# Kernel optimization log

Measured on AMD Instinct MI355X. Metric: run time of the kernel, lower is better.

## Reference

```python
import jax, jax.numpy as jnp
import numpy as np

EPS = 1e-3  # keras LayerNormalization default epsilon


def layer_norm(x, gamma, beta):
    mu = jnp.mean(x, axis=-1, keepdims=True)
    var = jnp.var(x, axis=-1, keepdims=True)
    return (x - mu) * jax.lax.rsqrt(var + EPS) * gamma + beta


def setup_inputs() -> dict:
    key = jax.random.key(0)
    ks = jax.random.split(key, 16)
    B, S, D = 8, 2048, 1024          # batch, seq, input_size
    P = 2 * D                        # up-projection dim (proj_factor=2)
    H = 1024                         # hidden = head_size(64) * num_heads(16)
    s = 0.02
    inp = {
        "x": jax.random.normal(ks[0], (B, S, D), jnp.float32),
        "ln1_g": jnp.ones((D,), jnp.float32),
        "ln1_b": jnp.zeros((D,), jnp.float32),
        "W_up": jax.random.normal(ks[1], (D, P), jnp.float32) * s,
        "b_up": jnp.zeros((P,), jnp.float32),
        "W_adj": jax.random.normal(ks[2], (P, H), jnp.float32) * s,
        "b_adj": jnp.zeros((H,), jnp.float32),
        "W_q": jax.random.normal(ks[3], (H, H), jnp.float32) * s,
        "b_q": jnp.zeros((H,), jnp.float32),
        "W_k": jax.random.normal(ks[4], (H, H), jnp.float32) * s,
        "b_k": jnp.zeros((H,), jnp.float32),
        "W_v": jax.random.normal(ks[5], (H, H), jnp.float32) * s,
        "b_v": jnp.zeros((H,), jnp.float32),
        "W_i": jax.random.normal(ks[6], (H, H), jnp.float32) * s,
        "b_i": jnp.zeros((H,), jnp.float32),
        "W_f": jax.random.normal(ks[7], (H, H), jnp.float32) * s,
        "b_f": jnp.zeros((H,), jnp.float32),
        "W_o": jax.random.normal(ks[8], (H, H), jnp.float32) * s,
        "b_o": jnp.zeros((H,), jnp.float32),
        "ln2_g": jnp.ones((H,), jnp.float32),
        "ln2_b": jnpos if False else jnp.zeros((H,), jnp.float32),
        "W_down": jax.random.normal(ks[9], (H, D), jnp.float32) * s,
        "b_down": jnp.zeros((D,), jnp.float32),
    }
    return inp


def reference(x, ln1_g, ln1_b, W_up, b_up, W_adj, b_adj,
              W_q, b_q, W_k, b_k, W_v, b_v,
              W_i, b_i, W_f, b_f, W_o, b_o,
              ln2_g, ln2_b, W_down, b_down):
    head_size = 64
    x_norm = layer_norm(x, ln1_g, ln1_b)
    x_up = x_norm @ W_up + b_up                      # [B,S,2D]
    x_adj = x_up @ W_adj + b_adj                     # [B,S,H]
    # BlockDiagonal layers: each block is a Dense over the FULL input,
    # concatenated -> equivalent to one [H,H] matmul with concatenated weights.
    q = x_adj @ W_q + b_q
    k = (x_adj @ W_k + b_k) / (head_size ** 0.5)
    v = x_adj @ W_v + b_v
    i_t = x_adj @ W_i + b_i
    f_t = x_adj @ W_f + b_f
    o = jax.nn.sigmoid(x_adj @ W_o + b_o)
    m_t = jnp.maximum(f_t, i_t)
    f = jnp.exp(f_t - m_t)                           # (i = exp(i_t - m_t) unused downstream)
    c_t = f * v * k
    h_t = o * (c_t * q) / jnp.maximum(jnp.abs(k * q), 1.0)
    out = layer_norm(h_t, ln2_g, ln2_b) * jax.nn.sigmoid(x_adj)
    out = out @ W_down + b_down
    return out + x
```

## Files before the change

kernel.cpp:

```cpp
#include <hip/hip_runtime.h>


typedef unsigned short u16;
typedef __attribute__((ext_vector_type(4))) unsigned short u16x4;
typedef __attribute__((ext_vector_type(8))) unsigned short u16x8;
typedef __attribute__((ext_vector_type(8))) __bf16 bf16x8;
typedef __attribute__((ext_vector_type(4))) float f32x4;

__device__ __forceinline__ float bf2f(u16 u) {
    union { unsigned int i; float f; } c; c.i = ((unsigned int)u) << 16; return c.f;
}
__device__ __forceinline__ u16 f2bf(float f) {
    union { float f; unsigned int i; } c; c.f = f;
    unsigned int lsb = (c.i >> 16) & 1u;
    c.i += 0x7fffu + lsb;
    return (u16)(c.i >> 16);
}
__device__ __forceinline__ float sigmoidf(float z) {
    return 1.0f / (1.0f + __expf(-z));
}

#define GLDS16(gp, lp)                                                        \
    __builtin_amdgcn_global_load_lds(                                         \
        (__attribute__((address_space(1))) void*)(void*)(gp),                 \
        (__attribute__((address_space(3))) void*)(lp), 16, 0, 0)

#define BM 128
#define BN 128
#define BK 32

template <int MODE>
__global__ __launch_bounds__(256) void gemm_bt(
    const u16* __restrict__ A, const u16* __restrict__ Bt,
    const float* __restrict__ bias, const float* __restrict__ resid,
    void* __restrict__ out, int M, int N, int K, float scale)
{
    __shared__ __align__(16) u16 As[2 * BM * BK];
    __shared__ __align__(16) u16 Bs[2 * BN * BK];

    const int tid  = threadIdx.x;
    const int lane = tid & 63;
    const int wave = tid >> 6;
    const int l15  = lane & 15;
    const int quad = lane >> 4;

    const long bm = (long)blockIdx.y * BM;
    const long bn = (long)blockIdx.x * BN;
    const int  wm = (wave >> 1) * 64;
    const int  wn = (wave & 1) * 64;

    f32x4 acc[4][4] = {};

    const int  r0 = tid >> 2;
    const int  ck = (((tid & 3) ^ ((tid >> 3) & 3)) * 8);
    const u16* ga0 = A  + (bm + r0) * (long)K + ck;
    const u16* gb0 = Bt + (bn + r0) * (long)K + ck;
    const int  ldst = wave * 512;

    auto stage = [&](int t_, int b_) {
        const long kof = (long)t_ * BK;
        u16* dA = &As[b_ * (BM * BK) + ldst];
        u16* dB = &Bs[b_ * (BN * BK) + ldst];
        GLDS16(ga0 + kof, dA);
        GLDS16(ga0 + kof + 64 * (long)K, dA + 2048);
        GLDS16(gb0 + kof, dB);
        GLDS16(gb0 + kof + 64 * (long)K, dB + 2048);
    };

    const int q8s = (quad ^ ((l15 >> 1) & 3)) * 8;
    const int nk  = K / BK;

    stage(0, 0);
    stage(1, 1);

    for (int t = 0; t < nk; ++t) {
        const int cur = t & 1;
        if (t + 1 < nk) asm volatile("s_waitcnt vmcnt(4)" ::: "memory");
        else            asm volatile("s_waitcnt vmcnt(0)" ::: "memory");
        __builtin_amdgcn_s_barrier();

        bf16x8 af[4], bfr[4];
#pragma unroll
        for (int t4 = 0; t4 < 4; ++t4) {
            af[t4]  = *(const bf16x8*)&As[cur * (BM * BK) + (wm + t4 * 16 + l15) * BK + q8s];
            bfr[t4] = *(const bf16x8*)&Bs[cur * (BN * BK) + (wn + t4 * 16 + l15) * BK + q8s];
        }
        asm volatile("s_waitcnt lgkmcnt(0)" ::: "memory");
        __builtin_amdgcn_s_barrier();
        if (t + 2 < nk) stage(t + 2, cur);

#pragma unroll
        for (int mt = 0; mt < 4; ++mt)
#pragma unroll
            for (int nt = 0; nt < 4; ++nt)
                acc[mt][nt] = __builtin_amdgcn_mfma_f32_16x16x32_bf16(
                    af[mt], bfr[nt], acc[mt][nt], 0, 0, 0);
    }

#pragma unroll
    for (int nt = 0; nt < 4; ++nt) {
        const long n  = bn + wn + nt * 16 + l15;
        const float bv = (MODE == 2) ? 0.0f : bias[n];
#pragma unroll
        for (int mt = 0; mt < 4; ++mt) {
            const long m0 = bm + wm + mt * 16 + quad * 4;
#pragma unroll
            for (int r = 0; r < 4; ++r) {
                const long idx = (m0 + r) * N + n;
                const float val = (acc[mt][nt][r] + bv) * scale;
                if (MODE == 1) ((float*)out)[idx] = val + resid[idx];
                else           ((u16*)out)[idx] = f2bf(val);
            }
        }
    }
}

__global__ __launch_bounds__(256) void gemm_gates(
    const u16* __restrict__ A, const u16* __restrict__ Wcat,
    const float* __restrict__ bq_, const float* __restrict__ bk_,
    const float* __restrict__ bv_, const float* __restrict__ bi_,
    const float* __restrict__ bf_, const float* __restrict__ bo_,
    u16* __restrict__ ht, int M, int N, int K)
{
    __shared__ __align__(16) u16 As[2 * 128 * 64];
    __shared__ __align__(16) u16 Bs[2 * 6 * 32 * 64];

    const int tid  = threadIdx.x;
    const int lane = tid & 63;
    const int wave = tid >> 6;
    const int l15  = lane & 15;
    const int quad = lane >> 4;

    const long bm = (long)blockIdx.y * 128;
    const long bn = (long)blockIdx.x * 32;

    f32x4 acc[6][4] = {};

    const int  rr = lane >> 3;
    const int  ck = (((lane & 7) ^ rr) * 8);

    const u16* gaj[4];
    int lAo[4];
#pragma unroll
    for (int j = 0; j < 4; ++j) {
        const int c = wave * 4 + j;
        gaj[j] = A + (bm + c * 8 + rr) * (long)K + ck;
        lAo[j] = c * 512;
    }
    const u16* gbj[6];
    int lBo[6];
#pragma unroll
    for (int j = 0; j < 6; ++j) {
        const int c = wave * 6 + j;
        const int g = c >> 2;
        const int r = (c & 3) * 8 + rr;
        gbj[j] = Wcat + ((long)g * 1024 + bn + r) * (long)K + ck;
        lBo[j] = c * 512;
    }

    auto stage = [&](int t_, int b_) {
        const long kof = (long)t_ * 64;
#pragma unroll
        for (int j = 0; j < 4; ++j)
            GLDS16(gaj[j] + kof, &As[b_ * 8192 + lAo[j]]);
#pragma unroll
        for (int j = 0; j < 6; ++j)
            GLDS16(gbj[j] + kof, &Bs[b_ * 12288 + lBo[j]]);
    };

    const int mh = (wave >> 1) * 64;
    const int nb = (wave & 1) * 16;
    const int l7 = l15 & 7;
    const int nk = K >> 6;

    stage(0, 0);
    stage(1, 1);

    for (int t = 0; t < nk; ++t) {
        const int cur = t & 1;
        if (t + 1 < nk) asm volatile("s_waitcnt vmcnt(10)" ::: "memory");
        else            asm volatile("s_waitcnt vmcnt(0)"  ::: "memory");
        __builtin_amdgcn_s_barrier();

        const int ab = cur * 8192;
        const int bb = cur * 12288;

        {
            const int so = (quad ^ l7) * 8;
            bf16x8 af[4];
#pragma unroll
            for (int t4 = 0; t4 < 4; ++t4)
                af[t4] = *(const bf16x8*)&As[ab + (mh + t4 * 16 + l15) * 64 + so];
#pragma unroll
            for (int g = 0; g < 6; ++g) {
                const bf16x8 bfrag =
                    *(const bf16x8*)&Bs[bb + (g * 32 + nb + l15) * 64 + so];
#pragma unroll
                for (int t4 = 0; t4 < 4; ++t4)
                    acc[g][t4] = __builtin_amdgcn_mfma_f32_16x16x32_bf16(
                        af[t4], bfrag, acc[g][t4], 0, 0, 0);
            }
        }
        bf16x8 af1[4], bf1[6];
        {
            const int so = ((4 + quad) ^ l7) * 8;
#pragma unroll
            for (int t4 = 0; t4 < 4; ++t4)
                af1[t4] = *(const bf16x8*)&As[ab + (mh + t4 * 16 + l15) * 64 + so];
#pragma unroll
            for (int g = 0; g < 6; ++g)
                bf1[g] = *(const bf16x8*)&Bs[bb + (g * 32 + nb + l15) * 64 + so];
        }
        asm volatile("s_waitcnt lgkmcnt(0)" ::: "memory");
        __builtin_amdgcn_s_barrier();
        if (t + 2 < nk) stage(t + 2, cur);

#pragma unroll
        for (int g = 0; g < 6; ++g)
#pragma unroll
            for (int t4 = 0; t4 < 4; ++t4)
                acc[g][t4] = __builtin_amdgcn_mfma_f32_16x16x32_bf16(
                    af1[t4], bf1[g], acc[g][t4], 0, 0, 0);
    }

    const long n = bn + nb + l15;
    const float bqn = bq_[n], bkn = bk_[n], bvn = bv_[n];
    const float bin = bi_[n], bfn = bf_[n], bon = bo_[n];
#pragma unroll
    for (int t = 0; t < 4; ++t) {
        const long m0 = bm + mh + t * 16 + quad * 4;
#pragma unroll
        for (int r = 0; r < 4; ++r) {
            const float qf = acc[0][t][r] + bqn;
            const float kf = (acc[1][t][r] + bkn) * 0.125f;
            const float vf = acc[2][t][r] + bvn;
            const float fi = acc[3][t][r] + bin;
            const float ff = acc[4][t][r] + bfn;
            const float osig = sigmoidf(acc[5][t][r] + bon);
            const float mx = fmaxf(ff, fi);
            const float fe = __expf(ff - mx);
            const float ct = fe * vf * kf;
            const float h  = osig * (ct * qf) / fmaxf(fabsf(kf * qf), 1.0f);
            ht[(m0 + r) * N + n] = f2bf(h);
        }
    }
}

__global__ __launch_bounds__(256) void ln_in_kernel(
    const float* __restrict__ x, const float* __restrict__ g,
    const float* __restrict__ b, u16* __restrict__ xn)
{
    const long row = blockIdx.x;
    const int  tid = threadIdx.x;
    const float4 v = ((const float4*)(x + row * 1024))[tid];
    float s  = v.x + v.y + v.z + v.w;
    float s2 = v.x * v.x + v.y * v.y + v.z * v.z + v.w * v.w;
#pragma unroll
    for (int off = 32; off > 0; off >>= 1) {
        s  += __shfl_down(s, off);
        s2 += __shfl_down(s2, off);
    }
    __shared__ float red[8];
    const int wave = tid >> 6;
    if ((tid & 63) == 0) { red[wave] = s; red[4 + wave] = s2; }
    __syncthreads();
    if (tid == 0) {
        const float S  = red[0] + red[1] + red[2] + red[3];
        const float S2 = red[4] + red[5] + red[6] + red[7];
        const float mu = S * (1.0f / 1024.0f);
        const float var = S2 * (1.0f / 1024.0f) - mu * mu;
        red[0] = mu; red[1] = rsqrtf(var + 1e-3f);
    }
    __syncthreads();
    const float mu = red[0], rstd = red[1];
    const int c = tid * 4;
    u16x4 o;
    o.x = f2bf((v.x - mu) * rstd * g[c + 0] + b[c + 0]);
    o.y = f2bf((v.y - mu) * rstd * g[c + 1] + b[c + 1]);
    o.z = f2bf((v.z - mu) * rstd * g[c + 2] + b[c + 2]);
    o.w = f2bf((v.w - mu) * rstd * g[c + 3] + b[c + 3]);
    *(u16x4*)(xn + row * 1024 + c) = o;
}

__global__ __launch_bounds__(256) void convT_kernel(
    const float* __restrict__ W, u16* __restrict__ Wt, int K, int N)
{
    __shared__ float t[32][33];
    const int tx = threadIdx.x & 31;
    const int ty = threadIdx.x >> 5;
    const long bn = (long)blockIdx.x * 32;
    const long bk = (long)blockIdx.y * 32;
#pragma unroll
    for (int j = 0; j < 4; ++j)
        t[ty + j * 8][tx] = W[(bk + ty + j * 8) * N + bn + tx];
    __syncthreads();
#pragma unroll
    for (int j = 0; j < 4; ++j)
        Wt[(bn + ty + j * 8) * K + bk + tx] = f2bf(t[tx][ty + j * 8]);
}

__global__ __launch_bounds__(256) void convB_kernel(
    const float* __restrict__ W, u16* __restrict__ Wb)
{
    const long i = ((long)blockIdx.x * 256 + threadIdx.x) * 4;
    const float4 v = *(const float4*)(W + i);
    u16x4 o;
    o.x = f2bf(v.x); o.y = f2bf(v.y); o.z = f2bf(v.z); o.w = f2bf(v.w);
    *(u16x4*)(Wb + i) = o;
}

__global__ __launch_bounds__(256) void bcomb_kernel(
    const u16* __restrict__ WadjT, const float* __restrict__ bup,
    const float* __restrict__ badj, float* __restrict__ bcomb)
{
    const long h = blockIdx.x;
    const int  tid = threadIdx.x;
    const int  p = tid * 8;
    const u16x8 w = *(const u16x8*)&WadjT[h * 2048 + p];
    float s = 0.0f;
#pragma unroll
    for (int j = 0; j < 8; ++j) s += bf2f(w[j]) * bup[p + j];
#pragma unroll
    for (int off = 32; off > 0; off >>= 1) s += __shfl_down(s, off);
    __shared__ float red[4];
    const int wave = tid >> 6;
    if ((tid & 63) == 0) red[wave] = s;
    __syncthreads();
    if (tid == 0)
        bcomb[h] = red[0] + red[1] + red[2] + red[3] + badj[h];
}

__global__ __launch_bounds__(256) void ln2_kernel(
    const u16* __restrict__ ht, const u16* __restrict__ xadj,
    const float* __restrict__ g2, const float* __restrict__ b2,
    u16* __restrict__ y)
{
    const long base = (long)blockIdx.x * 1024;
    const int  tid = threadIdx.x;
    const int  c = tid * 4;
    const u16x4 hv = *(const u16x4*)&ht[base + c];
    const u16x4 xv = *(const u16x4*)&xadj[base + c];

    float h[4];
    float s = 0.0f, s2 = 0.0f;
#pragma unroll
    for (int j = 0; j < 4; ++j) {
        h[j] = bf2f(hv[j]);
        s += h[j]; s2 += h[j] * h[j];
    }
#pragma unroll
    for (int off = 32; off > 0; off >>= 1) {
        s  += __shfl_down(s, off);
        s2 += __shfl_down(s2, off);
    }
    __shared__ float red[8];
    const int wave = tid >> 6;
    if ((tid & 63) == 0) { red[wave] = s; red[4 + wave] = s2; }
    __syncthreads();
    if (tid == 0) {
        const float S  = red[0] + red[1] + red[2] + red[3];
        const float S2 = red[4] + red[5] + red[6] + red[7];
        const float mu = S * (1.0f / 1024.0f);
        const float var = S2 * (1.0f / 1024.0f) - mu * mu;
        red[0] = mu; red[1] = rsqrtf(var + 1e-3f);
    }
    __syncthreads();
    const float mu = red[0], rstd = red[1];
    u16x4 o;
#pragma unroll
    for (int j = 0; j < 4; ++j)
        o[j] = f2bf(((h[j] - mu) * rstd * g2[c + j] + b2[c + j]) * sigmoidf(bf2f(xv[j])));
    *(u16x4*)&y[base + c] = o;
}

extern "C" void kernel_launch(void* const* d_in, const int* in_sizes, int n_in,
                              void* d_out, int out_size, void* d_ws, size_t ws_size,
                              hipStream_t stream)
{
    const float* x    = (const float*)d_in[0];
    const float* g1   = (const float*)d_in[1];
    const float* b1   = (const float*)d_in[2];
    const float* Wup  = (const float*)d_in[3];
    const float* bup  = (const float*)d_in[4];
    const float* Wadj = (const float*)d_in[5];
    const float* badj = (const float*)d_in[6];
    const float* Wq = (const float*)d_in[7];   const float* bq = (const float*)d_in[8];
    const float* Wk = (const float*)d_in[9];   const float* bk = (const float*)d_in[10];
    const float* Wv = (const float*)d_in[11];  const float* bv = (const float*)d_in[12];
    const float* Wi = (const float*)d_in[13];  const float* bi = (const float*)d_in[14];
    const float* Wf = (const float*)d_in[15];  const float* bf = (const float*)d_in[16];
    const float* Wo = (const float*)d_in[17];  const float* bo = (const float*)d_in[18];
    const float* g2 = (const float*)d_in[19];  const float* b2 = (const float*)d_in[20];
    const float* Wdn = (const float*)d_in[21]; const float* bdn = (const float*)d_in[22];

    const int M = 8 * 2048;
    const int D = 1024, P = 2048, H = 1024;

    char* ws = (char*)d_ws;
    const size_t MB = 1024 * 1024;
    u16* xn     = (u16*)(ws + 0);
    u16* htb    = (u16*)(ws + 0);
    u16* yb     = (u16*)(ws + 0);
    u16* WcombT = (u16*)(ws + 32 * MB);
    float* bcomb = (float*)(ws + 36 * MB);
    u16* xadj   = (u16*)(ws + 96 * MB);
    u16* Wup_bf = (u16*)(ws + 128 * MB);
    u16* WadjT  = (u16*)(ws + 132 * MB);
    u16* Wcat   = (u16*)(ws + 136 * MB);
    u16* WdnT   = (u16*)(ws + 148 * MB);

    ln_in_kernel<<<M, 256, 0, stream>>>(x, g1, b1, xn);

    convB_kernel<<<(D * P) / (256 * 4), 256, 0, stream>>>(Wup, Wup_bf);
    convT_kernel<<<dim3(H / 32, P / 32), 256, 0, stream>>>(Wadj, WadjT, P, H);
    convT_kernel<<<dim3(H / 32, H / 32), 256, 0, stream>>>(Wq, Wcat + 0 * H * H, H, H);
    convT_kernel<<<dim3(H / 32, H / 32), 256, 0, stream>>>(Wk, Wcat + 1 * H * H, H, H);
    convT_kernel<<<dim3(H / 32, H / 32), 256, 0, stream>>>(Wv, Wcat + 2 * H * H, H, H);
    convT_kernel<<<dim3(H / 32, H / 32), 256, 0, stream>>>(Wi, Wcat + 3 * H * H, H, H);
    convT_kernel<<<dim3(H / 32, H / 32), 256, 0, stream>>>(Wf, Wcat + 4 * H * H, H, H);
    convT_kernel<<<dim3(H / 32, H / 32), 256, 0, stream>>>(Wo, Wcat + 5 * H * H, H, H);
    convT_kernel<<<dim3(D / 32, H / 32), 256, 0, stream>>>(Wdn, WdnT, H, D);
    bcomb_kernel<<<H, 256, 0, stream>>>(WadjT, bup, badj, bcomb);

    gemm_bt<2><<<dim3(D / BN, H / BM), 256, 0, stream>>>(
        WadjT, Wup_bf, nullptr, nullptr, WcombT, H, D, P, 1.0f);

    gemm_bt<0><<<dim3(H / BN, M / BM), 256, 0, stream>>>(
        xn, WcombT, bcomb, nullptr, xadj, M, H, D, 1.0f);

    gemm_gates<<<dim3(H / 32, M / 128), 256, 0, stream>>>(
        xadj, Wcat, bq, bk, bv, bi, bf, bo, htb, M, H, H);

    ln2_kernel<<<M, 256, 0, stream>>>(htb, xadj, g2, b2, yb);

    gemm_bt<1><<<dim3(D / BN, M / BM), 256, 0, stream>>>(yb, WdnT, bdn, x, (float*)d_out, M, D, H, 1.0f);
}
```

Measured before the change: 569.1 us.

## Merge weight prep kernels into one launch and raise wave priority around MFMA loops

```diff
diff --git a/kernel.cpp b/kernel.cpp
--- a/kernel.cpp
+++ b/kernel.cpp
@@ -89,12 +89,14 @@
         __builtin_amdgcn_s_barrier();
         if (t + 2 < nk) stage(t + 2, cur);
 
+        __builtin_amdgcn_s_setprio(1);
 #pragma unroll
         for (int mt = 0; mt < 4; ++mt)
 #pragma unroll
             for (int nt = 0; nt < 4; ++nt)
                 acc[mt][nt] = __builtin_amdgcn_mfma_f32_16x16x32_bf16(
                     af[mt], bfr[nt], acc[mt][nt], 0, 0, 0);
+        __builtin_amdgcn_s_setprio(0);
     }
 
 #pragma unroll
@@ -191,6 +193,7 @@
 #pragma unroll
             for (int t4 = 0; t4 < 4; ++t4)
                 af[t4] = *(const bf16x8*)&As[ab + (mh + t4 * 16 + l15) * 64 + so];
+            __builtin_amdgcn_s_setprio(1);
 #pragma unroll
             for (int g = 0; g < 6; ++g) {
                 const bf16x8 bfrag =
@@ -200,6 +203,7 @@
                     acc[g][t4] = __builtin_amdgcn_mfma_f32_16x16x32_bf16(
                         af[t4], bfrag, acc[g][t4], 0, 0, 0);
             }
+            __builtin_amdgcn_s_setprio(0);
         }
         bf16x8 af1[4], bf1[6];
         {
@@ -215,12 +219,14 @@
         __builtin_amdgcn_s_barrier();
         if (t + 2 < nk) stage(t + 2, cur);
 
+        __builtin_amdgcn_s_setprio(1);
 #pragma unroll
         for (int g = 0; g < 6; ++g)
 #pragma unroll
             for (int t4 = 0; t4 < 4; ++t4)
                 acc[g][t4] = __builtin_amdgcn_mfma_f32_16x16x32_bf16(
                     af1[t4], bf1[g], acc[g][t4], 0, 0, 0);
+        __builtin_amdgcn_s_setprio(0);
     }
 
     const long n = bn + nb + l15;
@@ -282,14 +288,21 @@
     *(u16x4*)(xn + row * 1024 + c) = o;
 }
 
-__global__ __launch_bounds__(256) void convT_kernel(
-    const float* __restrict__ W, u16* __restrict__ Wt, int K, int N)
-{
-    __shared__ float t[32][33];
+struct PrepArgs {
+    const float *Wadj, *Wq, *Wk, *Wv, *Wi, *Wf, *Wo, *Wdn, *Wup;
+    const float *bup, *badj;
+    u16 *WadjT, *Wcat, *WdnT, *Wup_bf;
+    float *bcomb;
+};
+
+__device__ __forceinline__ void do_transpose(
+    const float* __restrict__ W, u16* __restrict__ Wt,
+    int K, int N, int bx, int by, float (&t)[32][33])
+{
     const int tx = threadIdx.x & 31;
     const int ty = threadIdx.x >> 5;
-    const long bn = (long)blockIdx.x * 32;
-    const long bk = (long)blockIdx.y * 32;
+    const long bn = (long)bx * 32;
+    const long bk = (long)by * 32;
 #pragma unroll
     for (int j = 0; j < 4; ++j)
         t[ty + j * 8][tx] = W[(bk + ty + j * 8) * N + bn + tx];
@@ -299,35 +312,46 @@
         Wt[(bn + ty + j * 8) * K + bk + tx] = f2bf(t[tx][ty + j * 8]);
 }
 
-__global__ __launch_bounds__(256) void convB_kernel(
-    const float* __restrict__ W, u16* __restrict__ Wb)
-{
-    const long i = ((long)blockIdx.x * 256 + threadIdx.x) * 4;
-    const float4 v = *(const float4*)(W + i);
-    u16x4 o;
-    o.x = f2bf(v.x); o.y = f2bf(v.y); o.z = f2bf(v.z); o.w = f2bf(v.w);
-    *(u16x4*)(Wb + i) = o;
-}
-
-__global__ __launch_bounds__(256) void bcomb_kernel(
-    const u16* __restrict__ WadjT, const float* __restrict__ bup,
-    const float* __restrict__ badj, float* __restrict__ bcomb)
-{
-    const long h = blockIdx.x;
-    const int  tid = threadIdx.x;
-    const int  p = tid * 8;
-    const u16x8 w = *(const u16x8*)&WadjT[h * 2048 + p];
-    float s = 0.0f;
-#pragma unroll
-    for (int j = 0; j < 8; ++j) s += bf2f(w[j]) * bup[p + j];
-#pragma unroll
-    for (int off = 32; off > 0; off >>= 1) s += __shfl_down(s, off);
-    __shared__ float red[4];
-    const int wave = tid >> 6;
-    if ((tid & 63) == 0) red[wave] = s;
-    __syncthreads();
-    if (tid == 0)
-        bcomb[h] = red[0] + red[1] + red[2] + red[3] + badj[h];
+__global__ __launch_bounds__(256) void prep_kernel(PrepArgs a)
+{
+    __shared__ float t[32][33];
+    int bid = blockIdx.x;
+    if (bid < 2048) {
+        do_transpose(a.Wadj, a.WadjT, 2048, 1024, bid & 31, bid >> 5, t);
+        return;
+    }
+    bid -= 2048;
+    if (bid < 6144) {
+        const int g = bid >> 10, tt = bid & 1023;
+        const float* Wg = g == 0 ? a.Wq : g == 1 ? a.Wk : g == 2 ? a.Wv
+                        : g == 3 ? a.Wi : g == 4 ? a.Wf : a.Wo;
+        do_transpose(Wg, a.Wcat + (long)g * 1024 * 1024, 1024, 1024,
+                     tt & 31, tt >> 5, t);
+        return;
+    }
+    bid -= 6144;
+    if (bid < 1024) {
+        do_transpose(a.Wdn, a.WdnT, 1024, 1024, bid & 31, bid >> 5, t);
+        return;
+    }
+    bid -= 1024;
+    if (bid < 2048) {
+        const long i = ((long)bid * 256 + threadIdx.x) * 4;
+        const float4 v = *(const float4*)(a.Wup + i);
+        u16x4 o;
+        o.x = f2bf(v.x); o.y = f2bf(v.y); o.z = f2bf(v.z); o.w = f2bf(v.w);
+        *(u16x4*)(a.Wup_bf + i) = o;
+        return;
+    }
+    bid -= 2048;
+    {
+        const int h = bid * 256 + threadIdx.x;
+        float s = 0.0f;
+#pragma unroll 8
+        for (int p = 0; p < 2048; ++p)
+            s += a.bup[p] * a.Wadj[(long)p * 1024 + h];
+        a.bcomb[h] = s + a.badj[h];
+    }
 }
 
 __global__ __launch_bounds__(256) void ln2_kernel(
@@ -411,16 +435,13 @@
 
     ln_in_kernel<<<M, 256, 0, stream>>>(x, g1, b1, xn);
 
-    convB_kernel<<<(D * P) / (256 * 4), 256, 0, stream>>>(Wup, Wup_bf);
-    convT_kernel<<<dim3(H / 32, P / 32), 256, 0, stream>>>(Wadj, WadjT, P, H);
-    convT_kernel<<<dim3(H / 32, H / 32), 256, 0, stream>>>(Wq, Wcat + 0 * H * H, H, H);
-    convT_kernel<<<dim3(H / 32, H / 32), 256, 0, stream>>>(Wk, Wcat + 1 * H * H, H, H);
-    convT_kernel<<<dim3(H / 32, H / 32), 256, 0, stream>>>(Wv, Wcat + 2 * H * H, H, H);
-    convT_kernel<<<dim3(H / 32, H / 32), 256, 0, stream>>>(Wi, Wcat + 3 * H * H, H, H);
-    convT_kernel<<<dim3(H / 32, H / 32), 256, 0, stream>>>(Wf, Wcat + 4 * H * H, H, H);
-    convT_kernel<<<dim3(H / 32, H / 32), 256, 0, stream>>>(Wo, Wcat + 5 * H * H, H, H);
-    convT_kernel<<<dim3(D / 32, H / 32), 256, 0, stream>>>(Wdn, WdnT, H, D);
-    bcomb_kernel<<<H, 256, 0, stream>>>(WadjT, bup, badj, bcomb);
+    PrepArgs pa;
+    pa.Wadj = Wadj; pa.Wq = Wq; pa.Wk = Wk; pa.Wv = Wv; pa.Wi = Wi;
+    pa.Wf = Wf; pa.Wo = Wo; pa.Wdn = Wdn; pa.Wup = Wup;
+    pa.bup = bup; pa.badj = badj;
+    pa.WadjT = WadjT; pa.Wcat = Wcat; pa.WdnT = WdnT; pa.Wup_bf = Wup_bf;
+    pa.bcomb = bcomb;
+    prep_kernel<<<11268, 256, 0, stream>>>(pa);
 
     gemm_bt<2><<<dim3(D / BN, H / BM), 256, 0, stream>>>(
         WadjT, Wup_bf, nullptr, nullptr, WcombT, H, D, P, 1.0f);
```

After: 646.5 us. 13.6% more time.
